# Kernel optimization log

Hardware: AMD Instinct MI355X
Metric: run time of the kernel (lower is better)

## Reference

```python
import jax, jax.numpy as jnp
import numpy as np

POWERS = (0, 1, 2)
IN_F, OUT_F = 64, 64
B, N, T = 8, 2048, 12


def setup_inputs() -> dict:
    key = jax.random.key(0)
    ks = jax.random.split(key, 8)
    inp = {
        "x": jax.random.normal(ks[0], (B, IN_F, N, T), dtype=jnp.float32),
        "adj": jax.random.uniform(ks[1], (B, N, N), dtype=jnp.float32),
    }
    # Xavier-uniform weights per adjacency power, zero biases (as in initialize_weights)
    limit = float(np.sqrt(6.0 / (IN_F + OUT_F)))
    for i, p in enumerate(POWERS):
        inp[f"W{p}"] = jax.random.uniform(ks[2 + i], (IN_F, OUT_F), jnp.float32, -limit, limit)
        inp[f"b{p}"] = jnp.zeros((OUT_F,), jnp.float32)
    return inp


def _gcn_conv(x, adj, W, b, a_power):
    # x: [B, F, N, T]; W: [F, O]; adj: [B, N, N]
    h = jnp.einsum('bfnt,fo->bont', x, W) + b[None, :, None, None]
    # repeated diffusion along node axis: h[f, n] <- sum_m adj[n, m] h[f, m]
    for _ in range(a_power):
        h = jnp.einsum('bnm,bomt->bont', adj, h)
    return jax.nn.leaky_relu(h)  # default negative_slope 0.01, same as torch


def reference(x, adj, W0, b0, W1, b1, W2, b2):
    params = {0: (W0, b0), 1: (W1, b1), 2: (W2, b2)}
    outs = [_gcn_conv(x, adj, params[p][0], params[p][1], p) for p in POWERS]
    return jnp.concatenate(outs, axis=1)  # [B, len(POWERS)*O, N, T]
```

## Files before the change

### kernel.cpp

```cpp
#include <hip/hip_runtime.h>

#define B_ 8
#define N_ 2048
#define T_ 12
#define F_ 64
#define NT 24576
#define CH 192
#define C_ 768

typedef __bf16 bf16x8 __attribute__((ext_vector_type(8)));
typedef float f32x4 __attribute__((ext_vector_type(4)));

typedef const __attribute__((address_space(1))) unsigned int as1_uint;
typedef __attribute__((address_space(3))) unsigned int as3_uint;

__device__ __forceinline__ void gload16(const void* g, void* l) {
  __builtin_amdgcn_global_load_lds((as1_uint*)g, (as3_uint*)l, 16, 0, 0);
}

__device__ __forceinline__ unsigned short f2bf(float f) {
  unsigned int u = __float_as_uint(f);
  u += 0x7FFFu + ((u >> 16) & 1u);
  return (unsigned short)(u >> 16);
}

__device__ __forceinline__ float bf2f(unsigned short u) {
  return __uint_as_float(((unsigned int)u) << 16);
}

__device__ __forceinline__ float leaky(float v) {
  return v >= 0.0f ? v : 0.01f * v;
}

__global__ __launch_bounds__(256) void convert_rs_k(const float* __restrict__ adj,
                                                    unsigned short* __restrict__ adjb,
                                                    float* __restrict__ rs1) {
  const int row = blockIdx.x;
  const int tid = threadIdx.x;
  const int lane = tid & 63;
  const int wave = tid >> 6;
  const float4* src = reinterpret_cast<const float4*>(adj + (size_t)row * N_);
  ushort4* dst = reinterpret_cast<ushort4*>(adjb + (size_t)row * N_);

  float s = 0.0f;
#pragma unroll
  for (int i = tid; i < 512; i += 256) {
    const float4 v = src[i];
    ushort4 u;
    u.x = f2bf(v.x); u.y = f2bf(v.y); u.z = f2bf(v.z); u.w = f2bf(v.w);
    dst[i] = u;
    s += v.x + v.y + v.z + v.w;
  }
#pragma unroll
  for (int o = 32; o; o >>= 1) s += __shfl_xor(s, o);
  __shared__ float red[4];
  if (lane == 0) red[wave] = s;
  __syncthreads();
  if (tid == 0) rs1[row] = red[0] + red[1] + red[2] + red[3];
}

__global__ __launch_bounds__(256) void rs2_k(const unsigned short* __restrict__ adjb,
                                             const float* __restrict__ rs1,
                                             float* __restrict__ rs2) {
  const int row = blockIdx.x;
  const int b = row >> 11;
  const int tid = threadIdx.x;
  const int lane = tid & 63;
  const int wave = tid >> 6;
  const ushort4* src = reinterpret_cast<const ushort4*>(adjb + (size_t)row * N_);
  const float* r1 = rs1 + ((size_t)b << 11);

  float s = 0.0f;
#pragma unroll
  for (int i = tid; i < 512; i += 256) {
    const ushort4 a = src[i];
    const int m = i * 4;
    s += bf2f(a.x) * r1[m] + bf2f(a.y) * r1[m + 1]
       + bf2f(a.z) * r1[m + 2] + bf2f(a.w) * r1[m + 3];
  }
#pragma unroll
  for (int o = 32; o; o >>= 1) s += __shfl_xor(s, o);
  __shared__ float red[4];
  if (lane == 0) red[wave] = s;
  __syncthreads();
  if (tid == 0) rs2[row] = red[0] + red[1] + red[2] + red[3];
}

__global__ __launch_bounds__(256) void convertX_k(const float* __restrict__ x,
                                                  unsigned short* __restrict__ Xt) {
  __shared__ float xl[T_][260];
  const int tid = threadIdx.x;
  const int n0 = blockIdx.x * 256;
  const int f = blockIdx.y;
  const int b = blockIdx.z;

  const float* src = x + (((size_t)b * F_ + f) * N_ + n0 + tid) * T_;
  float4 v0 = *reinterpret_cast<const float4*>(src);
  float4 v1 = *reinterpret_cast<const float4*>(src + 4);
  float4 v2 = *reinterpret_cast<const float4*>(src + 8);
  xl[0][tid] = v0.x;  xl[1][tid] = v0.y;  xl[2][tid] = v0.z;  xl[3][tid] = v0.w;
  xl[4][tid] = v1.x;  xl[5][tid] = v1.y;  xl[6][tid] = v1.z;  xl[7][tid] = v1.w;
  xl[8][tid] = v2.x;  xl[9][tid] = v2.y;  xl[10][tid] = v2.z; xl[11][tid] = v2.w;
  __syncthreads();
#pragma unroll
  for (int t = 0; t < T_; ++t)
    Xt[((size_t)b * C_ + f * T_ + t) * N_ + n0 + tid] = f2bf(xl[t][tid]);
}

__device__ __forceinline__ void stage_wt(const float* __restrict__ W,
                                         unsigned short* Wt, int tid) {
  const int f = tid >> 2;
  const int q = tid & 3;
  const float4* row = reinterpret_cast<const float4*>(W + f * 64 + q * 16);
#pragma unroll
  for (int v4 = 0; v4 < 4; ++v4) {
    float4 v = row[v4];
    const int ob = q * 16 + v4 * 4;
    Wt[(ob + 0) * 72 + f] = f2bf(v.x);
    Wt[(ob + 1) * 72 + f] = f2bf(v.y);
    Wt[(ob + 2) * 72 + f] = f2bf(v.z);
    Wt[(ob + 3) * 72 + f] = f2bf(v.w);
  }
}

__global__ __launch_bounds__(256) void p0_k(const float* __restrict__ x,
                                            const float* __restrict__ W0,
                                            const float* __restrict__ bia0,
                                            float* __restrict__ out) {
  __shared__ unsigned short Wt[64 * 72];
  __shared__ float bias[64];
  const int tid = threadIdx.x;
  stage_wt(W0, Wt, tid);
  if (tid < 64) bias[tid] = bia0[tid];
  __syncthreads();

  const int lane = tid & 63;
  const int wave = tid >> 6;
  const int b = blockIdx.y;
  const int e = blockIdx.x * 64 + wave * 16 + (lane & 15);
  const int fgrp = (lane >> 4) * 8;
  const float* xb = x + (size_t)b * F_ * NT;

  bf16x8 xf[2];
#pragma unroll
  for (int kf = 0; kf < 2; ++kf)
#pragma unroll
    for (int j = 0; j < 8; ++j)
      xf[kf][j] = (__bf16)xb[(size_t)(fgrp + kf * 32 + j) * NT + e];

  float* outb = out + (size_t)b * CH * NT;
#pragma unroll
  for (int ob = 0; ob < 4; ++ob) {
    f32x4 acc = {};
#pragma unroll
    for (int kf = 0; kf < 2; ++kf) {
      bf16x8 af = *reinterpret_cast<const bf16x8*>(
          &Wt[(ob * 16 + (lane & 15)) * 72 + kf * 32 + fgrp]);
      acc = __builtin_amdgcn_mfma_f32_16x16x32_bf16(af, xf[kf], acc, 0, 0, 0);
    }
#pragma unroll
    for (int r = 0; r < 4; ++r) {
      const int o = ob * 16 + (lane >> 4) * 4 + r;
      outb[(size_t)o * NT + e] = leaky(acc[r] + bias[o]);
    }
  }
}

__global__ __launch_bounds__(256) void pT_k(const unsigned short* __restrict__ Yt,
                                            const float* __restrict__ W,
                                            const float* __restrict__ bia,
                                            const float* __restrict__ rs,
                                            float* __restrict__ out,
                                            const int ocb) {
  __shared__ unsigned short Wt[64 * 72];
  __shared__ float bias[64];
  const int tid = threadIdx.x;
  stage_wt(W, Wt, tid);
  if (tid < 64) bias[tid] = bia[tid];
  __syncthreads();

  const int lane = tid & 63;
  const int wave = tid >> 6;
  const int b = blockIdx.y;
  const int n = blockIdx.x * 16 + (lane & 15);
  const int fgrp = (lane >> 4) * 8;
  const __bf16* Yb = reinterpret_cast<const __bf16*>(Yt + (size_t)b * C_ * N_);
  const float rsv = rs[((size_t)b << 11) + n];
  float* outb = out + (size_t)b * CH * NT;

#pragma unroll
  for (int it = 0; it < 3; ++it) {
    const int t = wave * 3 + it;

    bf16x8 xf[2];
#pragma unroll
    for (int kf = 0; kf < 2; ++kf)
#pragma unroll
      for (int j = 0; j < 8; ++j)
        xf[kf][j] = Yb[(size_t)((kf * 32 + fgrp + j) * T_ + t) * N_ + n];

#pragma unroll
    for (int ob = 0; ob < 4; ++ob) {
      f32x4 acc = {};
#pragma unroll
      for (int kf = 0; kf < 2; ++kf) {
        bf16x8 af = *reinterpret_cast<const bf16x8*>(
            &Wt[(ob * 16 + (lane & 15)) * 72 + kf * 32 + fgrp]);
        acc = __builtin_amdgcn_mfma_f32_16x16x32_bf16(af, xf[kf], acc, 0, 0, 0);
      }
#pragma unroll
      for (int r = 0; r < 4; ++r) {
        const int o = ob * 16 + (lane >> 4) * 4 + r;
        outb[(size_t)(ocb + o) * NT + n * T_ + t] = leaky(acc[r] + rsv * bias[o]);
      }
    }
  }
}

__global__ __launch_bounds__(256, 4) void gemmF_k(
    const unsigned short* __restrict__ adjb,
    const unsigned short* __restrict__ Bt,
    unsigned short* __restrict__ Ht)
{
  __shared__ __align__(16) unsigned short lds[14336];

  const int tid  = threadIdx.x;
  const int lane = tid & 63;
  const int wave = tid >> 6;
  const int wm = wave >> 1;
  const int wn = wave & 1;

  const int b  = blockIdx.x & 7;
  const int j  = blockIdx.x >> 3;
  const int n0 = (j & 15) * 128;
  const int c0 = (j >> 4) * 96;

  const unsigned short* A  = adjb + (size_t)b * N_ * N_;
  const unsigned short* Bm = Bt   + (size_t)b * C_ * N_;

  const int swz = ((lane & 7) ^ (lane >> 3)) * 8;
  const unsigned short* aSt = A + (size_t)(n0 + wave * 32 + (lane >> 3)) * N_ + swz;
  const unsigned short* bSt = Bm + (size_t)(c0 + wave * 24 + (lane >> 3)) * N_ + swz;

  const int lr15 = lane & 15;
  const int x7   = lane & 7;
  const int aBase = (wm * 64 + lr15) * 64;
  const int bBase = 8192 + (wn * 48 + lr15) * 64;

  f32x4 acc[4][3] = {};

#define STG(KT) \
  gload16(aSt + (KT) * 64,            lds + wave * 2048); \
  gload16(aSt + 8 * N_ + (KT) * 64,   lds + wave * 2048 + 512); \
  gload16(aSt + 16 * N_ + (KT) * 64,  lds + wave * 2048 + 1024); \
  gload16(aSt + 24 * N_ + (KT) * 64,  lds + wave * 2048 + 1536); \
  gload16(bSt + (KT) * 64,            lds + 8192 + wave * 1536); \
  gload16(bSt + 8 * N_ + (KT) * 64,   lds + 8192 + wave * 1536 + 512); \
  gload16(bSt + 16 * N_ + (KT) * 64,  lds + 8192 + wave * 1536 + 1024);

  STG(0)

#pragma unroll 1
  for (int kt = 0; kt < 32; ++kt) {
    __syncthreads();
#pragma unroll
    for (int kk = 0; kk < 2; ++kk) {
      const int g = ((kk * 4 + (lane >> 4)) ^ x7) * 8;
      bf16x8 af[4], bfv[3];
#pragma unroll
      for (int m = 0; m < 4; ++m)
        af[m] = *(const bf16x8*)(lds + aBase + m * 1024 + g);
#pragma unroll
      for (int nf = 0; nf < 3; ++nf)
        bfv[nf] = *(const bf16x8*)(lds + bBase + nf * 1024 + g);
#pragma unroll
      for (int m = 0; m < 4; ++m)
#pragma unroll
        for (int nf = 0; nf < 3; ++nf)
          acc[m][nf] = __builtin_amdgcn_mfma_f32_16x16x32_bf16(
              af[m], bfv[nf], acc[m][nf], 0, 0, 0);
    }
    __syncthreads();
    if (kt + 1 < 32) { STG(kt + 1) }
  }

  const int r4 = (lane >> 4) * 4;
  unsigned short* Hb = Ht + (size_t)b * C_ * N_;
#pragma unroll
  for (int m = 0; m < 4; ++m) {
#pragma unroll
    for (int nf = 0; nf < 3; ++nf) {
      const int c = c0 + wn * 48 + nf * 16 + lr15;
      const int nb = n0 + wm * 64 + m * 16 + r4;
      ushort4 u;
      u.x = f2bf(acc[m][nf][0]);
      u.y = f2bf(acc[m][nf][1]);
      u.z = f2bf(acc[m][nf][2]);
      u.w = f2bf(acc[m][nf][3]);
      *reinterpret_cast<ushort4*>(&Hb[(size_t)c * N_ + nb]) = u;
    }
  }
#undef STG
}

extern "C" void kernel_launch(void* const* d_in, const int* in_sizes, int n_in,
                              void* d_out, int out_size, void* d_ws, size_t ws_size,
                              hipStream_t stream) {
  const float* x   = (const float*)d_in[0];
  const float* adj = (const float*)d_in[1];
  const float* W0  = (const float*)d_in[2];
  const float* b0  = (const float*)d_in[3];
  const float* W1  = (const float*)d_in[4];
  const float* b1  = (const float*)d_in[5];
  const float* W2  = (const float*)d_in[6];
  const float* b2  = (const float*)d_in[7];
  float* out = (float*)d_out;

  char* ws = (char*)d_ws;
  unsigned short* adjb = (unsigned short*)ws;
  unsigned short* R1   = (unsigned short*)(ws + 67108864);
  unsigned short* R2   = (unsigned short*)(ws + 92274688);
  float* rs1 = (float*)(ws + 117440512);
  float* rs2 = (float*)(ws + 117506048);

  hipLaunchKernelGGL(convert_rs_k, dim3(B_ * N_), dim3(256), 0, stream,
                     adj, adjb, rs1);

  hipLaunchKernelGGL(convertX_k, dim3(N_ / 256, F_, B_), dim3(256), 0, stream,
                     x, R1);

  hipLaunchKernelGGL(p0_k, dim3(NT / 64, B_), dim3(256), 0, stream,
                     x, W0, b0, out);

  hipLaunchKernelGGL(gemmF_k, dim3(1024), dim3(256), 0, stream,
                     adjb, R1, R2);

  hipLaunchKernelGGL(rs2_k, dim3(B_ * N_), dim3(256), 0, stream,
                     adjb, rs1, rs2);

  hipLaunchKernelGGL(pT_k, dim3(N_ / 16, B_), dim3(256), 0, stream,
                     R2, W1, b1, rs1, out, 64);

  hipLaunchKernelGGL(gemmF_k, dim3(1024), dim3(256), 0, stream,
                     adjb, R2, R1);

  hipLaunchKernelGGL(pT_k, dim3(N_ / 16, B_), dim3(256), 0, stream,
                     R1, W2, b2, rs2, out, 128);
}
```

Baseline: 263.2 us.

## Enlarge adjacency GEMM tile to 128x192 and use 32x32x16 MFMA

The diffusion GEMM kernel now computes a 128x192 output tile per block instead of 128x96, which halves the grid and halves how often the adjacency tile is reloaded. It also switches from 16x16x32 to 32x32x16 bf16 MFMA, with a new LDS swizzle and a new epilogue layout. Each wave gets a larger accumulator footprint and occupancy drops to two blocks per CU. The result is fewer blocks (512 on a large CU count) and more register pressure, with less overlap between the global-to-LDS loads and compute.

```diff
diff --git a/kernel.cpp b/kernel.cpp
--- a/kernel.cpp
+++ b/kernel.cpp
@@ -10,6 +10,7 @@
 
 typedef __bf16 bf16x8 __attribute__((ext_vector_type(8)));
 typedef float f32x4 __attribute__((ext_vector_type(4)));
+typedef float f32x16 __attribute__((ext_vector_type(16)));
 
 typedef const __attribute__((address_space(1))) unsigned int as1_uint;
 typedef __attribute__((address_space(3))) unsigned int as3_uint;
@@ -217,12 +218,12 @@
   }
 }
 
-__global__ __launch_bounds__(256, 4) void gemmF_k(
+__global__ __launch_bounds__(256, 2) void gemmB_k(
     const unsigned short* __restrict__ adjb,
     const unsigned short* __restrict__ Bt,
     unsigned short* __restrict__ Ht)
 {
-  __shared__ __align__(16) unsigned short lds[14336];
+  __shared__ __align__(16) unsigned short lds[20480];
 
   const int tid  = threadIdx.x;
   const int lane = tid & 63;
@@ -233,30 +234,36 @@
   const int b  = blockIdx.x & 7;
   const int j  = blockIdx.x >> 3;
   const int n0 = (j & 15) * 128;
-  const int c0 = (j >> 4) * 96;
+  const int c0 = (j >> 4) * 192;
 
   const unsigned short* A  = adjb + (size_t)b * N_ * N_;
   const unsigned short* Bm = Bt   + (size_t)b * C_ * N_;
 
   const int swz = ((lane & 7) ^ (lane >> 3)) * 8;
   const unsigned short* aSt = A + (size_t)(n0 + wave * 32 + (lane >> 3)) * N_ + swz;
-  const unsigned short* bSt = Bm + (size_t)(c0 + wave * 24 + (lane >> 3)) * N_ + swz;
-
-  const int lr15 = lane & 15;
-  const int x7   = lane & 7;
-  const int aBase = (wm * 64 + lr15) * 64;
-  const int bBase = 8192 + (wn * 48 + lr15) * 64;
-
-  f32x4 acc[4][3] = {};
+  const unsigned short* bSt = Bm + (size_t)(c0 + wave * 48 + (lane >> 3)) * N_ + swz;
+
+  const int l31 = lane & 31;
+  const int x7  = lane & 7;
+  const int hi  = lane >> 5;
+  const int sh  = (lane >> 1) & 3;
+  const int e0  = hi ^ (x7 & 1);
+  const int aBase0 = (wm * 64 + l31) * 64;
+  const int bBase0 = 8192 + (wn * 96 + l31) * 64;
+
+  f32x16 acc[2][3] = {};
 
 #define STG(KT) \
   gload16(aSt + (KT) * 64,            lds + wave * 2048); \
   gload16(aSt + 8 * N_ + (KT) * 64,   lds + wave * 2048 + 512); \
   gload16(aSt + 16 * N_ + (KT) * 64,  lds + wave * 2048 + 1024); \
   gload16(aSt + 24 * N_ + (KT) * 64,  lds + wave * 2048 + 1536); \
-  gload16(bSt + (KT) * 64,            lds + 8192 + wave * 1536); \
-  gload16(bSt + 8 * N_ + (KT) * 64,   lds + 8192 + wave * 1536 + 512); \
-  gload16(bSt + 16 * N_ + (KT) * 64,  lds + 8192 + wave * 1536 + 1024);
+  gload16(bSt + (KT) * 64,            lds + 8192 + wave * 3072); \
+  gload16(bSt + 8 * N_ + (KT) * 64,   lds + 8192 + wave * 3072 + 512); \
+  gload16(bSt + 16 * N_ + (KT) * 64,  lds + 8192 + wave * 3072 + 1024); \
+  gload16(bSt + 24 * N_ + (KT) * 64,  lds + 8192 + wave * 3072 + 1536); \
+  gload16(bSt + 32 * N_ + (KT) * 64,  lds + 8192 + wave * 3072 + 2048); \
+  gload16(bSt + 40 * N_ + (KT) * 64,  lds + 8192 + wave * 3072 + 2560);
 
   STG(0)
 
@@ -264,40 +271,42 @@
   for (int kt = 0; kt < 32; ++kt) {
     __syncthreads();
 #pragma unroll
-    for (int kk = 0; kk < 2; ++kk) {
-      const int g = ((kk * 4 + (lane >> 4)) ^ x7) * 8;
-      bf16x8 af[4], bfv[3];
-#pragma unroll
-      for (int m = 0; m < 4; ++m)
-        af[m] = *(const bf16x8*)(lds + aBase + m * 1024 + g);
+    for (int s = 0; s < 4; ++s) {
+      const int ge = ((((s) ^ sh) << 1) | e0) * 8;
+      bf16x8 af[2], bfv[3];
+#pragma unroll
+      for (int m = 0; m < 2; ++m)
+        af[m] = *(const bf16x8*)(lds + aBase0 + m * 2048 + ge);
 #pragma unroll
       for (int nf = 0; nf < 3; ++nf)
-        bfv[nf] = *(const bf16x8*)(lds + bBase + nf * 1024 + g);
-#pragma unroll
-      for (int m = 0; m < 4; ++m)
+        bfv[nf] = *(const bf16x8*)(lds + bBase0 + nf * 2048 + ge);
+#pragma unroll
+      for (int m = 0; m < 2; ++m)
 #pragma unroll
         for (int nf = 0; nf < 3; ++nf)
-          acc[m][nf] = __builtin_amdgcn_mfma_f32_16x16x32_bf16(
+          acc[m][nf] = __builtin_amdgcn_mfma_f32_32x32x16_bf16(
               af[m], bfv[nf], acc[m][nf], 0, 0, 0);
     }
     __syncthreads();
     if (kt + 1 < 32) { STG(kt + 1) }
   }
 
-  const int r4 = (lane >> 4) * 4;
   unsigned short* Hb = Ht + (size_t)b * C_ * N_;
 #pragma unroll
-  for (int m = 0; m < 4; ++m) {
+  for (int m = 0; m < 2; ++m) {
 #pragma unroll
     for (int nf = 0; nf < 3; ++nf) {
-      const int c = c0 + wn * 48 + nf * 16 + lr15;
-      const int nb = n0 + wm * 64 + m * 16 + r4;
-      ushort4 u;
-      u.x = f2bf(acc[m][nf][0]);
-      u.y = f2bf(acc[m][nf][1]);
-      u.z = f2bf(acc[m][nf][2]);
-      u.w = f2bf(acc[m][nf][3]);
-      *reinterpret_cast<ushort4*>(&Hb[(size_t)c * N_ + nb]) = u;
+      const int c = c0 + wn * 96 + nf * 32 + l31;
+#pragma unroll
+      for (int q = 0; q < 4; ++q) {
+        const int nb = n0 + wm * 64 + m * 32 + q * 8 + 4 * hi;
+        ushort4 u;
+        u.x = f2bf(acc[m][nf][q * 4 + 0]);
+        u.y = f2bf(acc[m][nf][q * 4 + 1]);
+        u.z = f2bf(acc[m][nf][q * 4 + 2]);
+        u.w = f2bf(acc[m][nf][q * 4 + 3]);
+        *reinterpret_cast<ushort4*>(&Hb[(size_t)c * N_ + nb]) = u;
+      }
     }
   }
 #undef STG
@@ -332,7 +341,7 @@
   hipLaunchKernelGGL(p0_k, dim3(NT / 64, B_), dim3(256), 0, stream,
                      x, W0, b0, out);
 
-  hipLaunchKernelGGL(gemmF_k, dim3(1024), dim3(256), 0, stream,
+  hipLaunchKernelGGL(gemmB_k, dim3(512), dim3(256), 0, stream,
                      adjb, R1, R2);
 
   hipLaunchKernelGGL(rs2_k, dim3(B_ * N_), dim3(256), 0, stream,
@@ -341,7 +350,7 @@
   hipLaunchKernelGGL(pT_k, dim3(N_ / 16, B_), dim3(256), 0, stream,
                      R2, W1, b1, rs1, out, 64);
 
-  hipLaunchKernelGGL(gemmF_k, dim3(1024), dim3(256), 0, stream,
+  hipLaunchKernelGGL(gemmB_k, dim3(512), dim3(256), 0, stream,
                      adjb, R2, R1);
 
   hipLaunchKernelGGL(pT_k, dim3(N_ / 16, B_), dim3(256), 0, stream,
```

Measured after the change: 266.9 us. About the same (+1.4%).
